# Kernel tuning notes

Measured on AMD Instinct MI355X. Metric: run time of the kernel, lower is better.

The kernel has to match this reference:

```python
import jax, jax.numpy as jnp
import numpy as np

B, Q, K, DQ, DK = 4, 256, 1024, 256, 256


def setup_inputs() -> dict:
    key = jax.random.key(0)
    ks = jax.random.split(key, 7)
    q = jax.random.normal(ks[0], (B, Q, DQ), dtype=jnp.float32)
    k = jax.random.normal(ks[1], (B, K, DK), dtype=jnp.float32)
    v = jax.random.normal(ks[2], (B, K, DK), dtype=jnp.float32)
    mask = jax.random.randint(ks[3], (B, K), 0, 2).astype(bool)
    # torch Linear(in,out,bias=False): y = x @ W.T ; store as [in,out] for einsum
    Wq = jax.random.normal(ks[4], (DQ, DK), dtype=jnp.float32) / np.sqrt(DQ)
    Wk = jax.random.normal(ks[5], (DK, DK), dtype=jnp.float32) / np.sqrt(DK)
    wv = jax.random.normal(ks[6], (DK,), dtype=jnp.float32) / np.sqrt(DK)
    return {"q": q, "k": k, "v": v, "mask": mask, "Wq": Wq, "Wk": Wk, "wv": wv}


def reference(q, k, v, mask, Wq, Wk, wv):
    # Additive (Bahdanau) attention. Original redundantly projects repeated
    # copies; projecting once then broadcasting is the same math.
    qp = jnp.einsum('bqd,de->bqe', q, Wq)          # [B,Q,DK]
    kp = jnp.einsum('bkd,de->bke', k, Wk)          # [B,K,DK]
    h = jnp.tanh(qp[:, :, None, :] + kp[:, None, :, :])  # [B,Q,K,DK]
    scores = jnp.einsum('bqke,e->bqk', h, wv)      # [B,Q,K]
    scores = jnp.where(mask[:, None, :], scores, -jnp.inf)
    probs = jax.nn.softmax(scores, axis=-1)        # [B,Q,K]
    attended = jnp.einsum('bqk,bkd->bqd', probs, v)
    return attended
```

## Files before the change

kernel.cpp:

```cpp
#include <hip/hip_runtime.h>
#include <hip/hip_bf16.h>

#define B_ 4
#define Q_ 256
#define K_ 1024
#define D_ 256
#define NVPAD 1024
#define LOG2E 1.44269504f

__device__ __forceinline__ float fexp2(float x) {
    float r; asm("v_exp_f32 %0, %1" : "=v"(r) : "v"(x)); return r;
}
__device__ __forceinline__ float frcp(float x) {
    float r; asm("v_rcp_f32 %0, %1" : "=v"(r) : "v"(x)); return r;
}

__global__ void compact_kernel(const int* __restrict__ mask,
                               ushort* __restrict__ kidx,
                               short* __restrict__ slot_of,
                               int* __restrict__ nvalid) {
    const int b = blockIdx.x, lane = threadIdx.x;
    const int* m = mask + b * K_;
    const int base = lane * 16;
    int cnt = 0;
#pragma unroll
    for (int i = 0; i < 16; ++i) cnt += (m[base + i] != 0);
    int inc = cnt;
#pragma unroll
    for (int d = 1; d < 64; d <<= 1) {
        int tt = __shfl_up(inc, d);
        if (lane >= d) inc += tt;
    }
    const int total = __shfl(inc, 63);
    int pos = inc - cnt;
    ushort* kb = kidx + b * K_;
    short* so  = slot_of + b * K_;
    for (int i = 0; i < 16; ++i) {
        int kk = base + i;
        if (m[kk] != 0) { kb[pos] = (ushort)kk; so[kk] = (short)pos; ++pos; }
        else so[kk] = -1;
    }
    for (int j = total + lane; j < K_; j += 64) kb[j] = 0;
    if (lane == 0) nvalid[b] = total;
}

__global__ __launch_bounds__(256) void proj_kernel(const float* __restrict__ q,
                                                   const float* __restrict__ k,
                                                   const float* __restrict__ Wq,
                                                   const float* __restrict__ Wk,
                                                   const short* __restrict__ slot_of,
                                                   float* __restrict__ qpE,
                                                   float* __restrict__ kpC,
                                                   float scale) {
    const int t = threadIdx.x;
    const bool isQ = blockIdx.x < 16;
    const float* A; const float* W; int m0;
    if (isQ) { A = q; W = Wq; m0 = blockIdx.x * 64; }
    else     { A = k; W = Wk; m0 = (blockIdx.x - 16) * 64; }

    __shared__ float As[16][65];
    __shared__ float Ws[16][64];
    __shared__ short s_slot[64];
    if (!isQ && t < 64) s_slot[t] = slot_of[m0 + t];

    const int tx = t & 15, ty = t >> 4;
    const int n0 = blockIdx.y * 64;
    const int ar = t >> 2, ac = (t & 3) * 4;
    const int wr = t >> 4, wc = (t & 15) * 4;
    float c[4][4] = {};
    for (int kb = 0; kb < 256; kb += 16) {
        __syncthreads();
        float4 av = *(const float4*)(A + (size_t)(m0 + ar) * 256 + kb + ac);
        As[ac + 0][ar] = av.x; As[ac + 1][ar] = av.y;
        As[ac + 2][ar] = av.z; As[ac + 3][ar] = av.w;
        float4 wvv = *(const float4*)(W + (size_t)(kb + wr) * 256 + n0 + wc);
        wvv.x *= scale; wvv.y *= scale; wvv.z *= scale; wvv.w *= scale;
        *(float4*)(&Ws[wr][wc]) = wvv;
        __syncthreads();
#pragma unroll
        for (int kk = 0; kk < 16; ++kk) {
            float4 bv = *(const float4*)(&Ws[kk][tx * 4]);
#pragma unroll
            for (int i = 0; i < 4; ++i) {
                float a = As[kk][ty * 4 + i];
                c[i][0] = fmaf(a, bv.x, c[i][0]);
                c[i][1] = fmaf(a, bv.y, c[i][1]);
                c[i][2] = fmaf(a, bv.z, c[i][2]);
                c[i][3] = fmaf(a, bv.w, c[i][3]);
            }
        }
    }
    if (isQ) {
#pragma unroll
        for (int i = 0; i < 4; ++i) {
            float4 o = make_float4(fexp2(c[i][0]), fexp2(c[i][1]),
                                   fexp2(c[i][2]), fexp2(c[i][3]));
            *(float4*)(qpE + (size_t)(m0 + ty * 4 + i) * 256 + n0 + tx * 4) = o;
        }
    } else {
        const int b = m0 >> 10;
        float* kpCb = kpC + (size_t)b * 256 * NVPAD;
#pragma unroll
        for (int i = 0; i < 4; ++i) {
            const int sl = s_slot[ty * 4 + i];
            if (sl >= 0) {
#pragma unroll
                for (int j = 0; j < 4; ++j)
                    kpCb[(size_t)(n0 + tx * 4 + j) * NVPAD + sl] = fexp2(c[i][j]);
            }
        }
    }
}

__global__ __launch_bounds__(512, 2) void attn_kernel(const float* __restrict__ qpE,
                                                      const float* __restrict__ kpC,
                                                      const float* __restrict__ v,
                                                      const ushort* __restrict__ kidx_g,
                                                      const int* __restrict__ nvalid_g,
                                                      const float* __restrict__ wv,
                                                      float* __restrict__ out) {
    __shared__ float  s_qpA[2][256];
    __shared__ float  s_wv[256];
    __shared__ ushort s_kidx[1024];
    __shared__ float  s_sc[2][1024];
    __shared__ float4 s_pv[16][64];
    __shared__ float  s_inv[2];

    const int tid = threadIdx.x;

    int bid = blockIdx.x;
    bid = (bid & 7) * 64 + (bid >> 3);
    const int b  = bid >> 7;
    const int qi = bid & 127;
    const int q0 = qi * 2;

    const int nv = nvalid_g[b];

    if (tid < 64)        ((float4*)s_qpA[0])[tid]      = ((const float4*)(qpE + ((size_t)(b * Q_ + q0)     << 8)))[tid];
    else if (tid < 128)  ((float4*)s_qpA[1])[tid - 64] = ((const float4*)(qpE + ((size_t)(b * Q_ + q0 + 1) << 8)))[tid - 64];
    else if (tid < 192)  ((float4*)s_wv)[tid - 128]    = ((const float4*)wv)[tid - 128];
    s_kidx[tid]       = (tid < nv)       ? kidx_g[b * K_ + tid]       : (ushort)0;
    s_kidx[tid + 512] = (tid + 512 < nv) ? kidx_g[b * K_ + tid + 512] : (ushort)0;
    __syncthreads();

    const float* kpCb = kpC + (size_t)b * 256 * NVPAD;
    const float4* A0p = (const float4*)s_qpA[0];
    const float4* A1p = (const float4*)s_qpA[1];
    const float4* Wp  = (const float4*)s_wv;
    if (tid < nv) {
        float a0 = 0.f, a1 = 0.f;
        const float* col = kpCb + tid;
#pragma unroll 8
        for (int eg = 0; eg < 64; ++eg) {
            float4 A0 = A0p[eg], A1 = A1p[eg], W4 = Wp[eg];
            float Bx = col[(eg * 4 + 0) * NVPAD];
            float By = col[(eg * 4 + 1) * NVPAD];
            float Bz = col[(eg * 4 + 2) * NVPAD];
            float Bw = col[(eg * 4 + 3) * NVPAD];
            a0 = fmaf(W4.x, frcp(fmaf(A0.x, Bx, 1.f)), a0);
            a1 = fmaf(W4.x, frcp(fmaf(A1.x, Bx, 1.f)), a1);
            a0 = fmaf(W4.y, frcp(fmaf(A0.y, By, 1.f)), a0);
            a1 = fmaf(W4.y, frcp(fmaf(A1.y, By, 1.f)), a1);
            a0 = fmaf(W4.z, frcp(fmaf(A0.z, Bz, 1.f)), a0);
            a1 = fmaf(W4.z, frcp(fmaf(A1.z, Bz, 1.f)), a1);
            a0 = fmaf(W4.w, frcp(fmaf(A0.w, Bw, 1.f)), a0);
            a1 = fmaf(W4.w, frcp(fmaf(A1.w, Bw, 1.f)), a1);
        }
        s_sc[0][tid] = -2.f * a0;
        s_sc[1][tid] = -2.f * a1;
    }
    if (tid + 512 < nv) {
        float a0 = 0.f, a1 = 0.f;
        const float* col = kpCb + tid + 512;
#pragma unroll 8
        for (int eg = 0; eg < 64; ++eg) {
            float4 A0 = A0p[eg], A1 = A1p[eg], W4 = Wp[eg];
            float Bx = col[(eg * 4 + 0) * NVPAD];
            float By = col[(eg * 4 + 1) * NVPAD];
            float Bz = col[(eg * 4 + 2) * NVPAD];
            float Bw = col[(eg * 4 + 3) * NVPAD];
            a0 = fmaf(W4.x, frcp(fmaf(A0.x, Bx, 1.f)), a0);
            a1 = fmaf(W4.x, frcp(fmaf(A1.x, Bx, 1.f)), a1);
            a0 = fmaf(W4.y, frcp(fmaf(A0.y, By, 1.f)), a0);
            a1 = fmaf(W4.y, frcp(fmaf(A1.y, By, 1.f)), a1);
            a0 = fmaf(W4.z, frcp(fmaf(A0.z, Bz, 1.f)), a0);
            a1 = fmaf(W4.z, frcp(fmaf(A1.z, Bz, 1.f)), a1);
            a0 = fmaf(W4.w, frcp(fmaf(A0.w, Bw, 1.f)), a0);
            a1 = fmaf(W4.w, frcp(fmaf(A1.w, Bw, 1.f)), a1);
        }
        s_sc[0][tid + 512] = -2.f * a0;
        s_sc[1][tid + 512] = -2.f * a1;
    }
    __syncthreads();

    const int lane = tid & 63;
    const int wave = tid >> 6;
    if (wave < 2) {
        const int qq = wave;
        float mx = -3.0e38f;
        for (int j = lane; j < nv; j += 64) mx = fmaxf(mx, s_sc[qq][j]);
#pragma unroll
        for (int off = 32; off > 0; off >>= 1) mx = fmaxf(mx, __shfl_xor(mx, off));
        float sum = 0.f;
        for (int j = lane; j < nv; j += 64) {
            float e = fexp2((s_sc[qq][j] - mx) * LOG2E);
            s_sc[qq][j] = e;
            sum += e;
        }
#pragma unroll
        for (int off = 32; off > 0; off >>= 1) sum += __shfl_xor(sum, off);
        if (lane == 0) s_inv[qq] = frcp(sum);
    }
    __syncthreads();

    {
        const int dl = tid & 63;
        const int kq = tid >> 6;
        float4 o0 = {0, 0, 0, 0}, o1 = {0, 0, 0, 0};
        const float4* v4 = (const float4*)(v + ((size_t)b * K_ << 8));
        for (int k = kq; k < nv; k += 8) {
            int vr = s_kidx[k];
            float4 vv = v4[((size_t)vr << 6) + dl];
            float p0 = s_sc[0][k], p1 = s_sc[1][k];
            o0.x = fmaf(p0, vv.x, o0.x); o0.y = fmaf(p0, vv.y, o0.y);
            o0.z = fmaf(p0, vv.z, o0.z); o0.w = fmaf(p0, vv.w, o0.w);
            o1.x = fmaf(p1, vv.x, o1.x); o1.y = fmaf(p1, vv.y, o1.y);
            o1.z = fmaf(p1, vv.z, o1.z); o1.w = fmaf(p1, vv.w, o1.w);
        }
        s_pv[kq * 2 + 0][dl] = o0;
        s_pv[kq * 2 + 1][dl] = o1;
        __syncthreads();
        if (tid < 128) {
            const int qq = tid >> 6, c = tid & 63;
            float4 s = {0, 0, 0, 0};
#pragma unroll
            for (int g = 0; g < 8; ++g) {
                float4 x = s_pv[g * 2 + qq][c];
                s.x += x.x; s.y += x.y; s.z += x.z; s.w += x.w;
            }
            const float inv = s_inv[qq];
            s.x *= inv; s.y *= inv; s.z *= inv; s.w *= inv;
            ((float4*)out)[((size_t)(b * Q_ + q0 + qq) << 6) + c] = s;
        }
    }
}

extern "C" void kernel_launch(void* const* d_in, const int* in_sizes, int n_in,
                              void* d_out, int out_size, void* d_ws, size_t ws_size,
                              hipStream_t stream) {
    const float* q    = (const float*)d_in[0];
    const float* k    = (const float*)d_in[1];
    const float* v    = (const float*)d_in[2];
    const int*   mask = (const int*)d_in[3];
    const float* Wq   = (const float*)d_in[4];
    const float* Wk   = (const float*)d_in[5];
    const float* wv   = (const float*)d_in[6];
    float* out = (float*)d_out;

    float* qpE    = (float*)d_ws;
    float* kpC    = qpE + (size_t)B_ * Q_ * D_;
    ushort* kidx  = (ushort*)(kpC + (size_t)B_ * 256 * NVPAD);
    short* slot_of = (short*)(kidx + (size_t)B_ * K_);
    int* nvalid   = (int*)(slot_of + (size_t)B_ * K_);

    const float c2 = 2.885390082f;

    compact_kernel<<<dim3(B_), 64, 0, stream>>>(mask, kidx, slot_of, nvalid);
    proj_kernel<<<dim3(80, 4), 256, 0, stream>>>(q, k, Wq, Wk, slot_of, qpE, kpC, c2);
    attn_kernel<<<dim3(512), 512, 0, stream>>>(qpE, kpC, v, kidx, nvalid, wv, out);
}
```

Before: 67.35 us.

## Interleave projected keys as float4 groups and read query/weights directly from global

```diff
diff --git a/kernel.cpp b/kernel.cpp
--- a/kernel.cpp
+++ b/kernel.cpp
@@ -100,13 +100,14 @@
     } else {
         const int b = m0 >> 10;
         float* kpCb = kpC + (size_t)b * 256 * NVPAD;
+        const int e4 = (n0 + tx * 4) >> 2;
 #pragma unroll
         for (int i = 0; i < 4; ++i) {
             const int sl = s_slot[ty * 4 + i];
             if (sl >= 0) {
-#pragma unroll
-                for (int j = 0; j < 4; ++j)
-                    kpCb[(size_t)(n0 + tx * 4 + j) * NVPAD + sl] = fexp2(c[i][j]);
+                float4 o = make_float4(fexp2(c[i][0]), fexp2(c[i][1]),
+                                       fexp2(c[i][2]), fexp2(c[i][3]));
+                *(float4*)(kpCb + ((size_t)e4 * NVPAD + sl) * 4) = o;
             }
         }
     }
@@ -119,8 +120,6 @@
                                                       const int* __restrict__ nvalid_g,
                                                       const float* __restrict__ wv,
                                                       float* __restrict__ out) {
-    __shared__ float  s_qpA[2][256];
-    __shared__ float  s_wv[256];
     __shared__ ushort s_kidx[1024];
     __shared__ float  s_sc[2][1024];
     __shared__ float4 s_pv[16][64];
@@ -136,60 +135,33 @@
 
     const int nv = nvalid_g[b];
 
-    if (tid < 64)        ((float4*)s_qpA[0])[tid]      = ((const float4*)(qpE + ((size_t)(b * Q_ + q0)     << 8)))[tid];
-    else if (tid < 128)  ((float4*)s_qpA[1])[tid - 64] = ((const float4*)(qpE + ((size_t)(b * Q_ + q0 + 1) << 8)))[tid - 64];
-    else if (tid < 192)  ((float4*)s_wv)[tid - 128]    = ((const float4*)wv)[tid - 128];
     s_kidx[tid]       = (tid < nv)       ? kidx_g[b * K_ + tid]       : (ushort)0;
     s_kidx[tid + 512] = (tid + 512 < nv) ? kidx_g[b * K_ + tid + 512] : (ushort)0;
-    __syncthreads();
-
-    const float* kpCb = kpC + (size_t)b * 256 * NVPAD;
-    const float4* A0p = (const float4*)s_qpA[0];
-    const float4* A1p = (const float4*)s_qpA[1];
-    const float4* Wp  = (const float4*)s_wv;
-    if (tid < nv) {
+
+    const float4* Bp  = (const float4*)(kpC + (size_t)b * 256 * NVPAD);
+    const float4* A0p = (const float4*)(qpE + ((size_t)(b * Q_ + q0) << 8));
+    const float4* A1p = A0p + 64;
+    const float4* Wp  = (const float4*)wv;
+
+    for (int s0 = tid; s0 < nv; s0 += 512) {
         float a0 = 0.f, a1 = 0.f;
-        const float* col = kpCb + tid;
 #pragma unroll 8
         for (int eg = 0; eg < 64; ++eg) {
-            float4 A0 = A0p[eg], A1 = A1p[eg], W4 = Wp[eg];
-            float Bx = col[(eg * 4 + 0) * NVPAD];
-            float By = col[(eg * 4 + 1) * NVPAD];
-            float Bz = col[(eg * 4 + 2) * NVPAD];
-            float Bw = col[(eg * 4 + 3) * NVPAD];
-            a0 = fmaf(W4.x, frcp(fmaf(A0.x, Bx, 1.f)), a0);
-            a1 = fmaf(W4.x, frcp(fmaf(A1.x, Bx, 1.f)), a1);
-            a0 = fmaf(W4.y, frcp(fmaf(A0.y, By, 1.f)), a0);
-            a1 = fmaf(W4.y, frcp(fmaf(A1.y, By, 1.f)), a1);
-            a0 = fmaf(W4.z, frcp(fmaf(A0.z, Bz, 1.f)), a0);
-            a1 = fmaf(W4.z, frcp(fmaf(A1.z, Bz, 1.f)), a1);
-            a0 = fmaf(W4.w, frcp(fmaf(A0.w, Bw, 1.f)), a0);
-            a1 = fmaf(W4.w, frcp(fmaf(A1.w, Bw, 1.f)), a1);
-        }
-        s_sc[0][tid] = -2.f * a0;
-        s_sc[1][tid] = -2.f * a1;
-    }
-    if (tid + 512 < nv) {
-        float a0 = 0.f, a1 = 0.f;
-        const float* col = kpCb + tid + 512;
-#pragma unroll 8
-        for (int eg = 0; eg < 64; ++eg) {
-            float4 A0 = A0p[eg], A1 = A1p[eg], W4 = Wp[eg];
-            float Bx = col[(eg * 4 + 0) * NVPAD];
-            float By = col[(eg * 4 + 1) * NVPAD];
-            float Bz = col[(eg * 4 + 2) * NVPAD];
-            float Bw = col[(eg * 4 + 3) * NVPAD];
-            a0 = fmaf(W4.x, frcp(fmaf(A0.x, Bx, 1.f)), a0);
-            a1 = fmaf(W4.x, frcp(fmaf(A1.x, Bx, 1.f)), a1);
-            a0 = fmaf(W4.y, frcp(fmaf(A0.y, By, 1.f)), a0);
-            a1 = fmaf(W4.y, frcp(fmaf(A1.y, By, 1.f)), a1);
-            a0 = fmaf(W4.z, frcp(fmaf(A0.z, Bz, 1.f)), a0);
-            a1 = fmaf(W4.z, frcp(fmaf(A1.z, Bz, 1.f)), a1);
-            a0 = fmaf(W4.w, frcp(fmaf(A0.w, Bw, 1.f)), a0);
-            a1 = fmaf(W4.w, frcp(fmaf(A1.w, Bw, 1.f)), a1);
-        }
-        s_sc[0][tid + 512] = -2.f * a0;
-        s_sc[1][tid + 512] = -2.f * a1;
+            float4 Bv = Bp[(size_t)eg * NVPAD + s0];
+            float4 A0 = A0p[eg];
+            float4 A1 = A1p[eg];
+            float4 W4 = Wp[eg];
+            a0 = fmaf(W4.x, frcp(fmaf(A0.x, Bv.x, 1.f)), a0);
+            a1 = fmaf(W4.x, frcp(fmaf(A1.x, Bv.x, 1.f)), a1);
+            a0 = fmaf(W4.y, frcp(fmaf(A0.y, Bv.y, 1.f)), a0);
+            a1 = fmaf(W4.y, frcp(fmaf(A1.y, Bv.y, 1.f)), a1);
+            a0 = fmaf(W4.z, frcp(fmaf(A0.z, Bv.z, 1.f)), a0);
+            a1 = fmaf(W4.z, frcp(fmaf(A1.z, Bv.z, 1.f)), a1);
+            a0 = fmaf(W4.w, frcp(fmaf(A0.w, Bv.w, 1.f)), a0);
+            a1 = fmaf(W4.w, frcp(fmaf(A1.w, Bv.w, 1.f)), a1);
+        }
+        s_sc[0][s0] = -2.f * a0;
+        s_sc[1][s0] = -2.f * a1;
     }
     __syncthreads();
 
```

New measurement: 62.07 us. 7.8% less time.
